# Kernel tuning notes

Measured on AMD Instinct MI355X. Metric: run time of the kernel, lower is better.

The kernel has to match this reference:

```python
import jax, jax.numpy as jnp
import numpy as np

SEQ_LENGTH = 513
E = 512      # input_dim / embedding size
H = 1024     # hidden_dim
C = 512      # num_classes
B = 128      # batch


def setup_inputs() -> dict:
    key = jax.random.key(0)
    ks = jax.random.split(key, 12)

    def kaiming(k, shape):
        # kaiming_normal_ default: fan_in = shape[0] (fan computed on dim 1 of [out,in]; here params are [in,out] and torch uses fan_in=size(1)... torch fan_in for 2D = shape[1])
        fan_in = shape[1]
        std = np.sqrt(2.0 / fan_in)
        return jax.random.normal(k, shape, dtype=jnp.float32) * std

    inp = {
        "x": jax.random.randint(ks[0], (B, SEQ_LENGTH), 0, SEQ_LENGTH),
        "emb": jax.random.normal(ks[1], (SEQ_LENGTH, E), dtype=jnp.float32),
        "W_gx": kaiming(ks[2], (E, H)),
        "W_gh": kaiming(ks[3], (H, H)),
        "b_g": jnp.zeros((1, H), jnp.float32),
        "W_ix": kaiming(ks[4], (E, H)),
        "W_ih": kaiming(ks[5], (H, H)),
        "b_i": jnp.zeros((1, H), jnp.float32),
        "W_fx": kaiming(ks[6], (E, H)),
        "W_fh": kaiming(ks[7], (H, H)),
        "b_f": jnp.zeros((1, H), jnp.float32),
        "W_ox": kaiming(ks[8], (E, H)),
        "W_oh": kaiming(ks[9], (H, H)),
        "b_o": jnp.zeros((1, H), jnp.float32),
        "W_ph": kaiming(ks[10], (H, C)),
        "b_p": jnp.zeros((1, C), jnp.float32),
        "h_init": jnp.zeros((1, H), jnp.float32),
        "c_init": jnp.zeros((1, H), jnp.float32),
    }
    return inp


def reference(x, emb, W_gx, W_gh, b_g, W_ix, W_ih, b_i, W_fx, W_fh, b_f,
              W_ox, W_oh, b_o, W_ph, b_p, h_init, c_init):
    T = SEQ_LENGTH - 1  # module loops seq_length-1 steps
    embed_x = emb[x]                       # [B, SEQ_LENGTH, E]
    xs = jnp.swapaxes(embed_x[:, :T, :], 0, 1)  # [T, B, E]
    b = x.shape[0]
    h0 = jnp.broadcast_to(h_init, (b, H))
    c0 = jnp.broadcast_to(c_init, (b, H))

    def step(carry, e_t):
        h, c = carry
        g = jnp.tanh(e_t @ W_gx + h @ W_gh + b_g)
        i = jax.nn.sigmoid(e_t @ W_ix + h @ W_ih + b_i)
        f = jax.nn.sigmoid(e_t @ W_fx + h @ W_fh + b_f)
        o = jax.nn.sigmoid(e_t @ W_ox + h @ W_oh + b_o)
        c_new = g * i + c * f
        h_new = jnp.tanh(c_new) * o
        return (h_new, c_new), None

    (h_T, _), _ = jax.lax.scan(step, (h0, c0), xs)
    p_t = h_T @ W_ph + b_p                 # [B, C]
    return jax.nn.log_softmax(p_t, axis=1)
```

## Files before the change

### kernel.cpp

```cpp
#include <hip/hip_runtime.h>
#include <hip/hip_cooperative_groups.h>
#include <cmath>

namespace cg = cooperative_groups;

#define T_STEPS 512
#define NBLK 256

typedef _Float16 h8 __attribute__((ext_vector_type(8)));
typedef float f4 __attribute__((ext_vector_type(4)));
typedef int i32x4 __attribute__((ext_vector_type(4)));
typedef unsigned long long ull_t;

__device__ __forceinline__ float sigm(float v) { return 1.f / (1.f + __expf(-v)); }
__device__ __forceinline__ float tanh_fast(float v) { return 1.f - 2.f / (__expf(2.f * v) + 1.f); }

__global__ void pack_P(const float* __restrict__ emb,
                       const float* __restrict__ Wgx, const float* __restrict__ Wix,
                       const float* __restrict__ Wfx, const float* __restrict__ Wox,
                       const float* __restrict__ bg, const float* __restrict__ bi,
                       const float* __restrict__ bf_, const float* __restrict__ bo,
                       float* __restrict__ P) {
  __shared__ float es[8][512];
  const int vg = blockIdx.x;
  const int st = blockIdx.y;
  const int tid = threadIdx.x;
  for (int i = tid; i < 8 * 512; i += 256) {
    int vv = i >> 9, k = i & 511;
    int v = vg * 8 + vv;
    es[vv][k] = (v < 513) ? emb[v * 512 + k] : 0.f;
  }
  __syncthreads();
  const int c = st * 256 + tid;
  const int gate = c & 3, unit = c >> 2;
  const float* W = gate == 0 ? Wgx : gate == 1 ? Wix : gate == 2 ? Wfx : Wox;
  const float* bias = gate == 0 ? bg : gate == 1 ? bi : gate == 2 ? bf_ : bo;
  float acc[8];
  const float bv = bias[unit];
#pragma unroll
  for (int vv = 0; vv < 8; vv++) acc[vv] = bv;
  for (int k = 0; k < 512; k++) {
    float w = W[k * 1024 + unit];
#pragma unroll
    for (int vv = 0; vv < 8; vv++) acc[vv] += es[vv][k] * w;
  }
#pragma unroll
  for (int vv = 0; vv < 8; vv++) {
    int v = vg * 8 + vv;
    if (v < 513) P[(size_t)v * 4096 + c] = acc[vv];
  }
}

__global__ void pack_Wt(const float* __restrict__ Wgh, const float* __restrict__ Wih,
                        const float* __restrict__ Wfh, const float* __restrict__ Woh,
                        _Float16* __restrict__ Wt) {
  const int c = blockIdx.x;
  const int gate = c & 3, unit = c >> 2;
  const float* W = gate == 0 ? Wgh : gate == 1 ? Wih : gate == 2 ? Wfh : Woh;
  for (int k = threadIdx.x; k < 1024; k += 256)
    Wt[(size_t)c * 1024 + k] = (_Float16)W[k * 1024 + unit];
}

__launch_bounds__(512, 2)
__global__ void lstm_step_all(const int* __restrict__ x,
                              const float* __restrict__ P,
                              const _Float16* __restrict__ Wt,
                              _Float16* __restrict__ hbuf,
                              float* __restrict__ h32,
                              const float* __restrict__ h_init,
                              const float* __restrict__ c_init) {
  cg::grid_group grid = cg::this_grid();
  __shared__ _Float16 alds[16 * 1024];
  __shared__ float part[8 * 16 * 132];
  const int tid = threadIdx.x;
  const int blk = blockIdx.x;
  const int grp = blk & 7;
  const int sub = blk >> 3;
  const int lane = tid & 63;
  const int wid = tid >> 6;
  const int l15 = lane & 15;
  const int gg = lane >> 4;
  const int kg = gg * 8;
  const int colbase = sub * 128;
  const int ubase = sub * 32;
  const int rowbase = grp * 16;
  const int arow = tid >> 5;
  const int agb = tid & 31;

  h8 wfr[32];
  {
    const _Float16* wp = Wt + (size_t)(colbase + l15) * 1024 + wid * 128 + kg;
#pragma unroll
    for (int ct = 0; ct < 8; ct++)
#pragma unroll
      for (int ks = 0; ks < 4; ks++)
        wfr[ct * 4 + ks] = *(const h8*)(wp + (size_t)ct * 16 * 1024 + ks * 32);
  }

  if (tid < 128) {
    int r16 = tid >> 3, q = tid & 7;
    union { _Float16 h[4]; ull_t u; } pk;
#pragma unroll
    for (int u = 0; u < 4; u++) pk.h[u] = (_Float16)h_init[ubase + q * 4 + u];
    pk.u &= 0xFFFEFFFEFFFEFFFEull;
    *(ull_t*)&hbuf[(size_t)(rowbase + r16) * 1024 + ubase + q * 4] = pk.u;
    *(ull_t*)&hbuf[(size_t)(128 * 1024) + (size_t)(rowbase + r16) * 1024 + ubase + q * 4] =
        0x0001000100010001ull;
  }
  const int grow = tid >> 5;
  const int gu = tid & 31;
  float cst = c_init[ubase + gu];
  const int abase = arow * 1024 + ((agb ^ (arow & 7)) * 8);
  grid.sync();

  for (int t = 0; t < T_STEPS; t++) {
    const _Float16* hc = hbuf + (t & 1) * (128 * 1024);
    _Float16* hn = hbuf + ((t + 1) & 1) * (128 * 1024);

    const int xv = x[(rowbase + grow) * 513 + t];
    const float* prow = P + (size_t)xv * 4096 + colbase + gu * 4;
    f4 pv = *(const f4*)(prow);

    const int tagm = (int)(0x00010001u * (unsigned)((t >> 1) & 1));
    i32x4 av0, av1, av2, av3;
    {
      const _Float16* pbase = &hc[(size_t)(rowbase + arow) * 1024 + agb * 8];
      for (;;) {
        asm volatile("global_load_dwordx4 %0, %1, off sc0 sc1"
                     : "=v"(av0) : "v"(pbase) : "memory");
        asm volatile("global_load_dwordx4 %0, %1, off offset:512 sc0 sc1"
                     : "=v"(av1) : "v"(pbase) : "memory");
        asm volatile("global_load_dwordx4 %0, %1, off offset:1024 sc0 sc1"
                     : "=v"(av2) : "v"(pbase) : "memory");
        asm volatile("global_load_dwordx4 %0, %1, off offset:1536 sc0 sc1"
                     : "=v"(av3) : "v"(pbase) : "memory");
        asm volatile("s_waitcnt vmcnt(0)" ::: "memory");
        bool ok = true;
#pragma unroll
        for (int j = 0; j < 4; j++) {
          ok &= ((av0[j] & 0x00010001) == tagm);
          ok &= ((av1[j] & 0x00010001) == tagm);
          ok &= ((av2[j] & 0x00010001) == tagm);
          ok &= ((av3[j] & 0x00010001) == tagm);
        }
        if (ok) break;
        __builtin_amdgcn_s_sleep(1);
      }
    }
    __builtin_amdgcn_sched_barrier(0);
    *(i32x4*)&alds[abase] = av0;
    *(i32x4*)&alds[abase + 256] = av1;
    *(i32x4*)&alds[abase + 512] = av2;
    *(i32x4*)&alds[abase + 768] = av3;
    __syncthreads();

    h8 hfr[4];
#pragma unroll
    for (int ks = 0; ks < 4; ks++) {
      int g = wid * 16 + ks * 4 + gg;
      hfr[ks] = *(const h8*)&alds[l15 * 1024 + ((g ^ (l15 & 7)) * 8)];
    }

    f4 acc[8];
#pragma unroll
    for (int ct = 0; ct < 8; ct++) {
      acc[ct] = (f4){0.f, 0.f, 0.f, 0.f};
#pragma unroll
      for (int ks = 0; ks < 4; ks++)
        acc[ct] = __builtin_amdgcn_mfma_f32_16x16x32_f16(wfr[ct * 4 + ks], hfr[ks],
                                                         acc[ct], 0, 0, 0);
    }
#pragma unroll
    for (int ct = 0; ct < 8; ct++)
      *(f4*)&part[(wid * 16 + l15) * 132 + ct * 16 + 4 * gg] = acc[ct];
    __syncthreads();

    {
      f4 q = pv;
#pragma unroll
      for (int w = 0; w < 8; w++)
        q += *(const f4*)&part[(w * 16 + grow) * 132 + gu * 4];
      float g_ = tanh_fast(q[0]);
      float i_ = sigm(q[1]);
      float f_ = sigm(q[2]);
      float o_ = sigm(q[3]);
      cst = g_ * i_ + cst * f_;
      float hv = tanh_fast(cst) * o_;
      if (t == T_STEPS - 1) {
        h32[(size_t)(rowbase + grow) * 1024 + ubase + gu] = hv;
      } else {
        const unsigned tagn = (unsigned)(((t + 1) >> 1) & 1);
        union { _Float16 hh; unsigned short us; } cv;
        cv.hh = (_Float16)hv;
        unsigned v0 = ((unsigned)cv.us & 0xFFFEu) | tagn;
        unsigned v1 = (unsigned)__shfl_down((int)v0, 1);
        unsigned lo = (v0 & 0xffffu) | (v1 << 16);
        unsigned lo2 = (unsigned)__shfl_down((int)lo, 2);
        if ((gu & 3) == 0) {
          ull_t pv8 = (ull_t)lo | ((ull_t)lo2 << 32);
          __hip_atomic_store((ull_t*)&hn[(size_t)(rowbase + grow) * 1024 + ubase + gu],
                             pv8, __ATOMIC_RELAXED, __HIP_MEMORY_SCOPE_AGENT);
        }
      }
    }
  }
}

__global__ void proj(const float* __restrict__ h32, const float* __restrict__ Wph,
                     const float* __restrict__ bp, float* __restrict__ logits) {
  const int b = blockIdx.x >> 1;
  const int cc = (blockIdx.x & 1) * 256 + threadIdx.x;
  const float* hrow = h32 + b * 1024;
  float acc = bp[cc];
#pragma unroll 4
  for (int k = 0; k < 1024; k++) acc += hrow[k] * Wph[k * 512 + cc];
  logits[b * 512 + cc] = acc;
}

__global__ void lsm(const float* __restrict__ logits, float* __restrict__ out) {
  const int b = blockIdx.x;
  const int tid = threadIdx.x;
  __shared__ float sm[4];
  __shared__ float se[4];
  float v0 = logits[b * 512 + tid];
  float v1 = logits[b * 512 + 256 + tid];
  float m = fmaxf(v0, v1);
  for (int o = 1; o < 64; o <<= 1) m = fmaxf(m, __shfl_xor(m, o, 64));
  if ((tid & 63) == 0) sm[tid >> 6] = m;
  __syncthreads();
  m = fmaxf(fmaxf(sm[0], sm[1]), fmaxf(sm[2], sm[3]));
  float e = expf(v0 - m) + expf(v1 - m);
  for (int o = 1; o < 64; o <<= 1) e += __shfl_xor(e, o, 64);
  if ((tid & 63) == 0) se[tid >> 6] = e;
  __syncthreads();
  float ls = logf(se[0] + se[1] + se[2] + se[3]) + m;
  out[b * 512 + tid] = v0 - ls;
  out[b * 512 + 256 + tid] = v1 - ls;
}

extern "C" void kernel_launch(void* const* d_in, const int* in_sizes, int n_in,
                              void* d_out, int out_size, void* d_ws, size_t ws_size,
                              hipStream_t stream) {
  const int* x = (const int*)d_in[0];
  const float* emb = (const float*)d_in[1];
  const float* Wgx = (const float*)d_in[2];
  const float* Wgh = (const float*)d_in[3];
  const float* bg = (const float*)d_in[4];
  const float* Wix = (const float*)d_in[5];
  const float* Wih = (const float*)d_in[6];
  const float* bi = (const float*)d_in[7];
  const float* Wfx = (const float*)d_in[8];
  const float* Wfh = (const float*)d_in[9];
  const float* bf = (const float*)d_in[10];
  const float* Wox = (const float*)d_in[11];
  const float* Woh = (const float*)d_in[12];
  const float* bo = (const float*)d_in[13];
  const float* Wph = (const float*)d_in[14];
  const float* bp = (const float*)d_in[15];
  const float* h_init = (const float*)d_in[16];
  const float* c_init = (const float*)d_in[17];

  char* ws = (char*)d_ws;
  float* P = (float*)ws;
  _Float16* Wt = (_Float16*)(ws + 8519680);
  _Float16* hbuf = (_Float16*)(ws + 8519680 + 8388608);
  float* h32 = (float*)(ws + 8519680 + 8388608 + 524288);
  float* logits = (float*)(ws + 8519680 + 8388608 + 524288 + 524288);

  pack_P<<<dim3(65, 16), 256, 0, stream>>>(emb, Wgx, Wix, Wfx, Wox, bg, bi, bf, bo, P);
  pack_Wt<<<4096, 256, 0, stream>>>(Wgh, Wih, Wfh, Woh, Wt);

  void* args[] = {(void*)&x, (void*)&P, (void*)&Wt, (void*)&hbuf,
                  (void*)&h32, (void*)&h_init, (void*)&c_init};
  hipLaunchCooperativeKernel((void*)lstm_step_all, dim3(NBLK), dim3(512), args, 0, stream);

  proj<<<256, 256, 0, stream>>>(h32, Wph, bp, logits);
  lsm<<<128, 256, 0, stream>>>(logits, (float*)d_out);
}
```

Measured before the change: 1.387 ms.

## Load h fragments directly into MFMA registers, drop LDS staging and one barrier

```diff
diff --git a/kernel.cpp b/kernel.cpp
--- a/kernel.cpp
+++ b/kernel.cpp
@@ -70,8 +70,7 @@
                               const float* __restrict__ h_init,
                               const float* __restrict__ c_init) {
   cg::grid_group grid = cg::this_grid();
-  __shared__ _Float16 alds[16 * 1024];
-  __shared__ float part[8 * 16 * 132];
+  __shared__ float part[2][8 * 16 * 132];
   const int tid = threadIdx.x;
   const int blk = blockIdx.x;
   const int grp = blk & 7;
@@ -84,8 +83,6 @@
   const int colbase = sub * 128;
   const int ubase = sub * 32;
   const int rowbase = grp * 16;
-  const int arow = tid >> 5;
-  const int agb = tid & 31;
 
   h8 wfr[32];
   {
@@ -110,29 +107,29 @@
   const int grow = tid >> 5;
   const int gu = tid & 31;
   float cst = c_init[ubase + gu];
-  const int abase = arow * 1024 + ((agb ^ (arow & 7)) * 8);
   grid.sync();
 
   for (int t = 0; t < T_STEPS; t++) {
     const _Float16* hc = hbuf + (t & 1) * (128 * 1024);
     _Float16* hn = hbuf + ((t + 1) & 1) * (128 * 1024);
+    const int p = t & 1;
 
     const int xv = x[(rowbase + grow) * 513 + t];
     const float* prow = P + (size_t)xv * 4096 + colbase + gu * 4;
     f4 pv = *(const f4*)(prow);
 
+    i32x4 av0, av1, av2, av3;
     const int tagm = (int)(0x00010001u * (unsigned)((t >> 1) & 1));
-    i32x4 av0, av1, av2, av3;
     {
-      const _Float16* pbase = &hc[(size_t)(rowbase + arow) * 1024 + agb * 8];
+      const _Float16* pbase = &hc[(size_t)(rowbase + l15) * 1024 + wid * 128 + kg];
       for (;;) {
         asm volatile("global_load_dwordx4 %0, %1, off sc0 sc1"
                      : "=v"(av0) : "v"(pbase) : "memory");
-        asm volatile("global_load_dwordx4 %0, %1, off offset:512 sc0 sc1"
+        asm volatile("global_load_dwordx4 %0, %1, off offset:64 sc0 sc1"
                      : "=v"(av1) : "v"(pbase) : "memory");
-        asm volatile("global_load_dwordx4 %0, %1, off offset:1024 sc0 sc1"
+        asm volatile("global_load_dwordx4 %0, %1, off offset:128 sc0 sc1"
                      : "=v"(av2) : "v"(pbase) : "memory");
-        asm volatile("global_load_dwordx4 %0, %1, off offset:1536 sc0 sc1"
+        asm volatile("global_load_dwordx4 %0, %1, off offset:192 sc0 sc1"
                      : "=v"(av3) : "v"(pbase) : "memory");
         asm volatile("s_waitcnt vmcnt(0)" ::: "memory");
         bool ok = true;
@@ -143,43 +140,33 @@
           ok &= ((av2[j] & 0x00010001) == tagm);
           ok &= ((av3[j] & 0x00010001) == tagm);
         }
-        if (ok) break;
+        if (__ballot(ok) == ~0ull) break;
         __builtin_amdgcn_s_sleep(1);
       }
     }
     __builtin_amdgcn_sched_barrier(0);
-    *(i32x4*)&alds[abase] = av0;
-    *(i32x4*)&alds[abase + 256] = av1;
-    *(i32x4*)&alds[abase + 512] = av2;
-    *(i32x4*)&alds[abase + 768] = av3;
-    __syncthreads();
-
-    h8 hfr[4];
-#pragma unroll
-    for (int ks = 0; ks < 4; ks++) {
-      int g = wid * 16 + ks * 4 + gg;
-      hfr[ks] = *(const h8*)&alds[l15 * 1024 + ((g ^ (l15 & 7)) * 8)];
-    }
+    union { i32x4 i; h8 h; } hf0, hf1, hf2, hf3;
+    hf0.i = av0; hf1.i = av1; hf2.i = av2; hf3.i = av3;
 
     f4 acc[8];
 #pragma unroll
     for (int ct = 0; ct < 8; ct++) {
       acc[ct] = (f4){0.f, 0.f, 0.f, 0.f};
-#pragma unroll
-      for (int ks = 0; ks < 4; ks++)
-        acc[ct] = __builtin_amdgcn_mfma_f32_16x16x32_f16(wfr[ct * 4 + ks], hfr[ks],
-                                                         acc[ct], 0, 0, 0);
+      acc[ct] = __builtin_amdgcn_mfma_f32_16x16x32_f16(wfr[ct * 4 + 0], hf0.h, acc[ct], 0, 0, 0);
+      acc[ct] = __builtin_amdgcn_mfma_f32_16x16x32_f16(wfr[ct * 4 + 1], hf1.h, acc[ct], 0, 0, 0);
+      acc[ct] = __builtin_amdgcn_mfma_f32_16x16x32_f16(wfr[ct * 4 + 2], hf2.h, acc[ct], 0, 0, 0);
+      acc[ct] = __builtin_amdgcn_mfma_f32_16x16x32_f16(wfr[ct * 4 + 3], hf3.h, acc[ct], 0, 0, 0);
     }
 #pragma unroll
     for (int ct = 0; ct < 8; ct++)
-      *(f4*)&part[(wid * 16 + l15) * 132 + ct * 16 + 4 * gg] = acc[ct];
+      *(f4*)&part[p][(wid * 16 + l15) * 132 + ct * 16 + 4 * gg] = acc[ct];
     __syncthreads();
 
     {
       f4 q = pv;
 #pragma unroll
       for (int w = 0; w < 8; w++)
-        q += *(const f4*)&part[(w * 16 + grow) * 132 + gu * 4];
+        q += *(const f4*)&part[p][(w * 16 + grow) * 132 + gu * 4];
       float g_ = tanh_fast(q[0]);
       float i_ = sigm(q[1]);
       float f_ = sigm(q[2]);
```

Measured after the change: 1.889 ms. +36.2%, slower.
